# Performance work log

Hardware: AMD Instinct MI355X
Metric: run time of the kernel (lower is better)

The kernel has to match this reference:

```python
import jax, jax.numpy as jnp
import numpy as np

N = 50000      # nodes
E = 800000     # edges (before self-loops)
IN = 256
HID = 256
OUT = 128
D = 4
K = 4
K1 = 8
NUM_KS = K1 * ((1 << K) - 1)   # 120 centroids
S = HID // D                   # sub-dim per quantization slice
TAU = 1.0


def setup_inputs() -> dict:
    key = jax.random.key(0)
    ks = jax.random.split(key, 9)
    x = jax.random.normal(ks[0], (N, IN), jnp.float32)
    edge_index = jax.random.randint(ks[1], (2, E), 0, N, dtype=jnp.int64)
    def lin(k, fan_in, fan_out):
        return jax.random.normal(k, (fan_in, fan_out), jnp.float32) / np.float32(np.sqrt(fan_in))
    W0 = lin(ks[2], IN, HID); b0 = jnp.zeros((HID,), jnp.float32)
    W1 = lin(ks[3], HID, HID); b1 = jnp.zeros((HID,), jnp.float32)
    W2 = lin(ks[4], HID, OUT); b2 = jnp.zeros((OUT,), jnp.float32)
    # kaiming_normal on (NUM_KS, HID): std = sqrt(2 / fan_in), fan_in = HID
    centroids = jax.random.normal(ks[5], (NUM_KS, HID), jnp.float32) * np.float32(np.sqrt(2.0 / HID))
    return dict(x=x, edge_index=edge_index, W0=W0, b0=b0, W1=W1, b1=b1, W2=W2, b2=b2,
                centroids=centroids)


def gcn_conv(x, W, b, src, dst):
    # PyG GCNConv: add self-loops, symmetric normalization, aggregate at target
    n = x.shape[0]
    loops = jnp.arange(n, dtype=src.dtype)
    s2 = jnp.concatenate([src, loops])
    d2 = jnp.concatenate([dst, loops])
    deg = jax.ops.segment_sum(jnp.ones_like(d2, x.dtype), d2, num_segments=n)
    dinv = jnp.where(deg > 0, jax.lax.rsqrt(deg), 0.0)
    norm = dinv[s2] * dinv[d2]                      # [E+n]
    xw = x @ W                                      # [n, out]
    out = jax.ops.segment_sum(xw[s2] * norm[:, None], d2, num_segments=n)
    return out + b


def quantize(H, C):
    # H: [n, HID], C: [NUM_KS, HID]
    n = H.shape[0]
    Hr = H.reshape(n, D, S)
    Cr = C.reshape(NUM_KS, D, S)
    # products[n,k,d] = sum_s H[n,d,s] * C[k,d,s]
    prods = jnp.einsum('nds,kds->nkd', Hr, Cr) / TAU   # [n, NUM_KS, D]
    soft_l, hard_l, prob_l = [], [], []
    off = 0
    d_idx = jnp.arange(D)[None, :]
    for j in range(K):                 # K fixed small groups of sizes k_1<<j
        m = K1 << j
        sl = prods[:, off:off + m, :]                  # [n, m, D]
        p = jax.nn.softmax(sl, axis=1)                 # scatter_softmax within group
        Cg = Cr[off:off + m]                           # [m, D, S]
        soft_l.append(jnp.einsum('nmd,mds->nds', p, Cg))
        idx = jnp.argmax(sl, axis=1)                   # [n, D] scatter_max within group
        hard_l.append(Cg[idx, d_idx, :])               # [n, D, S]
        prob_l.append(p)
        off += m
    soft = jnp.stack(soft_l, 1).reshape(n, K, HID)
    hard = jnp.stack(hard_l, 1).reshape(n, K, HID)
    q = jax.lax.stop_gradient(hard - soft) + soft      # straight-through
    balance = jnp.concatenate(prob_l, 1).sum(0) / n    # [NUM_KS, D]
    k_blns = jnp.concatenate([jnp.full((K1 << j,), 1.0 / (K1 << j), jnp.float32) for j in range(K)])
    target = jnp.broadcast_to(k_blns[:, None], (NUM_KS, D))
    reg = jnp.linalg.norm(balance - target)
    pred = jnp.max(q, axis=1)                          # [n, HID]
    return pred, reg


def reference(x, edge_index, W0, b0, W1, b1, W2, b2, centroids):
    src, dst = edge_index[0], edge_index[1]
    h = jax.nn.leaky_relu(gcn_conv(x, W0, b0, src, dst), negative_slope=0.5)
    h = jax.nn.leaky_relu(gcn_conv(h, W1, b1, src, dst), negative_slope=0.5)
    pred, reg = quantize(h, centroids)
    h = h + pred
    out = gcn_conv(h, W2, b2, src, dst)
    return out, reg
```

## Files before the change

### kernel.cpp

```cpp
#include <hip/hip_runtime.h>
#include <math.h>



__global__ void k_init(int* cnt, int* cursor, int* counter, float* balance, int n) {
    int i = blockIdx.x * blockDim.x + threadIdx.x;
    if (i < n) { cnt[i] = 0; cursor[i] = 0; }
    if (i < 480) balance[i] = 0.f;
    if (i == 0) *counter = 0;
}

__global__ void k_count(const int* __restrict__ dst, int* __restrict__ cnt, int e) {
    int i = blockIdx.x * blockDim.x + threadIdx.x;
    if (i < e) atomicAdd(&cnt[dst[i]], 1);
}

__global__ void k_dinv(const int* __restrict__ cnt, float* __restrict__ dinv, int n) {
    int i = blockIdx.x * blockDim.x + threadIdx.x;
    if (i < n) dinv[i] = rsqrtf((float)cnt[i] + 1.0f);
}

__global__ void k_alloc(const int* __restrict__ cnt, int* __restrict__ row_start,
                        int* __restrict__ counter, int n) {
    int i = blockIdx.x * blockDim.x + threadIdx.x;
    if (i < n) row_start[i] = atomicAdd(counter, cnt[i]);
}

__global__ void k_fill(const int* __restrict__ src, const int* __restrict__ dst,
                       const float* __restrict__ dinv, const int* __restrict__ row_start,
                       int* __restrict__ cursor, int* __restrict__ csr_src,
                       float* __restrict__ csr_norm, int e) {
    int i = blockIdx.x * blockDim.x + threadIdx.x;
    if (i >= e) return;
    int s = src[i], d = dst[i];
    int slot = atomicAdd(&cursor[d], 1);
    int idx = row_start[d] + slot;
    csr_src[idx] = s;
    csr_norm[idx] = dinv[s] * dinv[d];
}


typedef short bf16x8 __attribute__((ext_vector_type(8)));
typedef float f32x4 __attribute__((ext_vector_type(4)));

__device__ __forceinline__ unsigned short bf16_rne(float a) {
    unsigned u = __builtin_bit_cast(unsigned, a);
    return (unsigned short)((u + 0x7FFFu + ((u >> 16) & 1u)) >> 16);
}
__device__ __forceinline__ float bf16_to_f(unsigned short h) {
    return __builtin_bit_cast(float, (unsigned)h << 16);
}

__global__ __launch_bounds__(256, 3) void k_gemm_mfma(const float* __restrict__ A,
                                                      const float* __restrict__ B,
                                                      float* __restrict__ C,
                                                      int M, int N) {
    constexpr int K = 256;
    __shared__ unsigned short Ash[128 * 40];
    __shared__ unsigned short Asl[128 * 40];
    __shared__ unsigned short Bsh[128 * 40];
    __shared__ unsigned short Bsl[128 * 40];
    const int tid = threadIdx.x;
    const int bm = blockIdx.x * 128;
    const int bn = blockIdx.y * 128;
    const int wave = tid >> 6, lane = tid & 63;
    const int wr = wave >> 1, wc = wave & 1;
    const int lr = lane & 15, lk = lane >> 4;

    f32x4 acc[4][4] = {};

    for (int k0 = 0; k0 < K; k0 += 32) {
#pragma unroll
        for (int it = 0; it < 4; ++it) {
            int q = it * 256 + tid;
            int row = q >> 3, kq = q & 7;
            float4 v = make_float4(0.f, 0.f, 0.f, 0.f);
            if (bm + row < M) v = *(const float4*)(A + (size_t)(bm + row) * K + k0 + kq * 4);
            float e[4] = {v.x, v.y, v.z, v.w};
            unsigned hh[4], ll[4];
#pragma unroll
            for (int t = 0; t < 4; ++t) {
                unsigned short h = bf16_rne(e[t]);
                unsigned short l = bf16_rne(e[t] - bf16_to_f(h));
                hh[t] = h; ll[t] = l;
            }
            unsigned off = row * 40 + kq * 4;
            *(uint2*)&Ash[off] = make_uint2(hh[0] | (hh[1] << 16), hh[2] | (hh[3] << 16));
            *(uint2*)&Asl[off] = make_uint2(ll[0] | (ll[1] << 16), ll[2] | (ll[3] << 16));
        }
#pragma unroll
        for (int it = 0; it < 4; ++it) {
            int q = it * 256 + tid;
            int k = q >> 5, nq = q & 31;
            float4 v = *(const float4*)(B + (size_t)(k0 + k) * N + bn + nq * 4);
            float e[4] = {v.x, v.y, v.z, v.w};
#pragma unroll
            for (int t = 0; t < 4; ++t) {
                unsigned short h = bf16_rne(e[t]);
                unsigned short l = bf16_rne(e[t] - bf16_to_f(h));
                Bsh[(nq * 4 + t) * 40 + k] = h;
                Bsl[(nq * 4 + t) * 40 + k] = l;
            }
        }
        __syncthreads();

        bf16x8 ah[4], al[4], bh[4], bl[4];
#pragma unroll
        for (int i = 0; i < 4; ++i) {
            unsigned off = (wr * 64 + i * 16 + lr) * 40 + lk * 8;
            ah[i] = *(bf16x8*)&Ash[off];
            al[i] = *(bf16x8*)&Asl[off];
        }
#pragma unroll
        for (int j = 0; j < 4; ++j) {
            unsigned off = (wc * 64 + j * 16 + lr) * 40 + lk * 8;
            bh[j] = *(bf16x8*)&Bsh[off];
            bl[j] = *(bf16x8*)&Bsl[off];
        }
#pragma unroll
        for (int i = 0; i < 4; ++i)
#pragma unroll
            for (int j = 0; j < 4; ++j) {
                acc[i][j] = __builtin_amdgcn_mfma_f32_16x16x32_bf16(al[i], bh[j], acc[i][j], 0, 0, 0);
                acc[i][j] = __builtin_amdgcn_mfma_f32_16x16x32_bf16(ah[i], bl[j], acc[i][j], 0, 0, 0);
                acc[i][j] = __builtin_amdgcn_mfma_f32_16x16x32_bf16(ah[i], bh[j], acc[i][j], 0, 0, 0);
            }
        __syncthreads();
    }

#pragma unroll
    for (int i = 0; i < 4; ++i) {
        int rbase = bm + wr * 64 + i * 16 + lk * 4;
#pragma unroll
        for (int r = 0; r < 4; ++r) {
            int row = rbase + r;
            if (row < M) {
#pragma unroll
                for (int j = 0; j < 4; ++j)
                    C[(size_t)row * N + bn + wc * 64 + j * 16 + lr] = acc[i][j][r];
            }
        }
    }
}


template <bool RELU>
__global__ __launch_bounds__(256, 4) void k_agg4(const float* __restrict__ xw,
                                                 const float* __restrict__ dinv,
                                                 const int* __restrict__ csr_src,
                                                 const float* __restrict__ csr_norm,
                                                 const int* __restrict__ row_start,
                                                 const int* __restrict__ cnt,
                                                 const float* __restrict__ bias,
                                                 float* __restrict__ out, int n) {
    int node = blockIdx.x * 4 + (threadIdx.x >> 6);
    if (node >= n) return;
    int lane = threadIdx.x & 63;
    int c = lane * 4;
    float di = dinv[node];
    float4 self = *(const float4*)(xw + (size_t)node * 256 + c);
    float4 bv = *(const float4*)(bias + c);
    float sw = di * di;
    float ax = self.x * sw + bv.x;
    float ay = self.y * sw + bv.y;
    float az = self.z * sw + bv.z;
    float aw = self.w * sw + bv.w;
    int st = row_start[node];
    int m = cnt[node];
    for (int t0 = 0; t0 < m; t0 += 64) {
        int rem = m - t0;
        int cnt_i = rem < 64 ? rem : 64;
        int idx_l = 0;
        float nrm_l = 0.f;
        if (lane < cnt_i) {
            idx_l = csr_src[st + t0 + lane];
            nrm_l = csr_norm[st + t0 + lane];
        }
        int t = 0;
        for (; t + 8 <= cnt_i; t += 8) {
            const float* p0 = xw + (size_t)__shfl(idx_l, t + 0, 64) * 256 + c;
            const float* p1 = xw + (size_t)__shfl(idx_l, t + 1, 64) * 256 + c;
            const float* p2 = xw + (size_t)__shfl(idx_l, t + 2, 64) * 256 + c;
            const float* p3 = xw + (size_t)__shfl(idx_l, t + 3, 64) * 256 + c;
            const float* p4 = xw + (size_t)__shfl(idx_l, t + 4, 64) * 256 + c;
            const float* p5 = xw + (size_t)__shfl(idx_l, t + 5, 64) * 256 + c;
            const float* p6 = xw + (size_t)__shfl(idx_l, t + 6, 64) * 256 + c;
            const float* p7 = xw + (size_t)__shfl(idx_l, t + 7, 64) * 256 + c;
            float4 v0 = *(const float4*)p0;
            float4 v1 = *(const float4*)p1;
            float4 v2 = *(const float4*)p2;
            float4 v3 = *(const float4*)p3;
            float4 v4 = *(const float4*)p4;
            float4 v5 = *(const float4*)p5;
            float4 v6 = *(const float4*)p6;
            float4 v7 = *(const float4*)p7;
            float w0 = __shfl(nrm_l, t + 0, 64);
            float w1 = __shfl(nrm_l, t + 1, 64);
            float w2 = __shfl(nrm_l, t + 2, 64);
            float w3 = __shfl(nrm_l, t + 3, 64);
            float w4 = __shfl(nrm_l, t + 4, 64);
            float w5 = __shfl(nrm_l, t + 5, 64);
            float w6 = __shfl(nrm_l, t + 6, 64);
            float w7 = __shfl(nrm_l, t + 7, 64);
            ax += v0.x * w0; ay += v0.y * w0; az += v0.z * w0; aw += v0.w * w0;
            ax += v1.x * w1; ay += v1.y * w1; az += v1.z * w1; aw += v1.w * w1;
            ax += v2.x * w2; ay += v2.y * w2; az += v2.z * w2; aw += v2.w * w2;
            ax += v3.x * w3; ay += v3.y * w3; az += v3.z * w3; aw += v3.w * w3;
            ax += v4.x * w4; ay += v4.y * w4; az += v4.z * w4; aw += v4.w * w4;
            ax += v5.x * w5; ay += v5.y * w5; az += v5.z * w5; aw += v5.w * w5;
            ax += v6.x * w6; ay += v6.y * w6; az += v6.z * w6; aw += v6.w * w6;
            ax += v7.x * w7; ay += v7.y * w7; az += v7.z * w7; aw += v7.w * w7;
        }
        for (; t < cnt_i; ++t) {
            int s = __shfl(idx_l, t, 64);
            float w = __shfl(nrm_l, t, 64);
            float4 v = *(const float4*)(xw + (size_t)s * 256 + c);
            ax += v.x * w; ay += v.y * w; az += v.z * w; aw += v.w * w;
        }
    }
    if (RELU) {
        ax = ax > 0.f ? ax : 0.5f * ax;
        ay = ay > 0.f ? ay : 0.5f * ay;
        az = az > 0.f ? az : 0.5f * az;
        aw = aw > 0.f ? aw : 0.5f * aw;
    }
    *(float4*)(out + (size_t)node * 256 + c) = make_float4(ax, ay, az, aw);
}

__global__ __launch_bounds__(256, 4) void k_agg2(const float* __restrict__ xw,
                                                 const float* __restrict__ dinv,
                                                 const int* __restrict__ csr_src,
                                                 const float* __restrict__ csr_norm,
                                                 const int* __restrict__ row_start,
                                                 const int* __restrict__ cnt,
                                                 const float* __restrict__ bias,
                                                 float* __restrict__ out, int n) {
    int node = blockIdx.x * 4 + (threadIdx.x >> 6);
    if (node >= n) return;
    int lane = threadIdx.x & 63;
    int c = lane * 2;
    float di = dinv[node];
    float2 self = *(const float2*)(xw + (size_t)node * 128 + c);
    float2 bv = *(const float2*)(bias + c);
    float sw = di * di;
    float ax = self.x * sw + bv.x;
    float ay = self.y * sw + bv.y;
    int st = row_start[node];
    int m = cnt[node];
    for (int t0 = 0; t0 < m; t0 += 64) {
        int rem = m - t0;
        int cnt_i = rem < 64 ? rem : 64;
        int idx_l = 0;
        float nrm_l = 0.f;
        if (lane < cnt_i) {
            idx_l = csr_src[st + t0 + lane];
            nrm_l = csr_norm[st + t0 + lane];
        }
        int t = 0;
        for (; t + 8 <= cnt_i; t += 8) {
            const float* p0 = xw + (size_t)__shfl(idx_l, t + 0, 64) * 128 + c;
            const float* p1 = xw + (size_t)__shfl(idx_l, t + 1, 64) * 128 + c;
            const float* p2 = xw + (size_t)__shfl(idx_l, t + 2, 64) * 128 + c;
            const float* p3 = xw + (size_t)__shfl(idx_l, t + 3, 64) * 128 + c;
            const float* p4 = xw + (size_t)__shfl(idx_l, t + 4, 64) * 128 + c;
            const float* p5 = xw + (size_t)__shfl(idx_l, t + 5, 64) * 128 + c;
            const float* p6 = xw + (size_t)__shfl(idx_l, t + 6, 64) * 128 + c;
            const float* p7 = xw + (size_t)__shfl(idx_l, t + 7, 64) * 128 + c;
            float2 v0 = *(const float2*)p0;
            float2 v1 = *(const float2*)p1;
            float2 v2 = *(const float2*)p2;
            float2 v3 = *(const float2*)p3;
            float2 v4 = *(const float2*)p4;
            float2 v5 = *(const float2*)p5;
            float2 v6 = *(const float2*)p6;
            float2 v7 = *(const float2*)p7;
            float w0 = __shfl(nrm_l, t + 0, 64);
            float w1 = __shfl(nrm_l, t + 1, 64);
            float w2 = __shfl(nrm_l, t + 2, 64);
            float w3 = __shfl(nrm_l, t + 3, 64);
            float w4 = __shfl(nrm_l, t + 4, 64);
            float w5 = __shfl(nrm_l, t + 5, 64);
            float w6 = __shfl(nrm_l, t + 6, 64);
            float w7 = __shfl(nrm_l, t + 7, 64);
            ax += v0.x * w0; ay += v0.y * w0;
            ax += v1.x * w1; ay += v1.y * w1;
            ax += v2.x * w2; ay += v2.y * w2;
            ax += v3.x * w3; ay += v3.y * w3;
            ax += v4.x * w4; ay += v4.y * w4;
            ax += v5.x * w5; ay += v5.y * w5;
            ax += v6.x * w6; ay += v6.y * w6;
            ax += v7.x * w7; ay += v7.y * w7;
        }
        for (; t < cnt_i; ++t) {
            int s = __shfl(idx_l, t, 64);
            float w = __shfl(nrm_l, t, 64);
            float2 v = *(const float2*)(xw + (size_t)s * 128 + c);
            ax += v.x * w; ay += v.y * w;
        }
    }
    *(float2*)(out + (size_t)node * 128 + c) = make_float2(ax, ay);
}


__global__ __launch_bounds__(256, 4) void k_quant4(const float* __restrict__ h2,
                                                   const float* __restrict__ cent,
                                                   float* __restrict__ h3,
                                                   float* __restrict__ balance_g, int n) {
    __shared__ float As[32 * 132];
    __shared__ float Bs[32 * 132];
    __shared__ float bal4[4 * 128];
    __shared__ int km_ls[128 * 4];
    const int tid = threadIdx.x;
    const int n0 = blockIdx.x * 128;
    const int d = blockIdx.y;
    const int ty = tid >> 4, tx = tid & 15;
    const int wave = tid >> 6, lane = tid & 63;

    int gid, base, sz;
    if (tx == 0)       { gid = 0; base = 0;  sz = 1; }
    else if (tx <= 2)  { gid = 1; base = 1;  sz = 2; }
    else if (tx <= 6)  { gid = 2; base = 3;  sz = 4; }
    else if (tx <= 14) { gid = 3; base = 7;  sz = 8; }
    else               { gid = 0; base = 15; sz = 0; }
    const int l = tx - base;
    const int segbase = lane & 48;

    {
        int k = tid >> 3, r = tid & 7;
        int col = (r < 4) ? (60 + r) : (120 + r);
        Bs[k * 132 + col] = 0.f;
    }

    float acc[8][8] = {};
    for (int c0 = 0; c0 < 64; c0 += 32) {
#pragma unroll
        for (int it = 0; it < 4; ++it) {
            int q = it * 256 + tid;
            int row = q >> 3, k4 = q & 7;
            float4 v = make_float4(0.f, 0.f, 0.f, 0.f);
            if (n0 + row < n)
                v = *(const float4*)(h2 + (size_t)(n0 + row) * 256 + d * 64 + c0 + k4 * 4);
            As[(k4 * 4 + 0) * 132 + row] = v.x;
            As[(k4 * 4 + 1) * 132 + row] = v.y;
            As[(k4 * 4 + 2) * 132 + row] = v.z;
            As[(k4 * 4 + 3) * 132 + row] = v.w;
        }
#pragma unroll
        for (int it = 0; it < 4; ++it) {
            int q = it * 256 + tid;
            if (q < 960) {
                int c = q >> 3, k4 = q & 7;
                float4 v = *(const float4*)(cent + (size_t)c * 256 + d * 64 + c0 + k4 * 4);
                int col = ((c >> 3) << 2) + (((c >> 2) & 1) << 6) + (c & 3);
                Bs[(k4 * 4 + 0) * 132 + col] = v.x;
                Bs[(k4 * 4 + 1) * 132 + col] = v.y;
                Bs[(k4 * 4 + 2) * 132 + col] = v.z;
                Bs[(k4 * 4 + 3) * 132 + col] = v.w;
            }
        }
        __syncthreads();
#pragma unroll 4
        for (int k = 0; k < 32; ++k) {
            float4 a0 = *(const float4*)&As[k * 132 + ty * 8];
            float4 a1 = *(const float4*)&As[k * 132 + ty * 8 + 4];
            float4 b0 = *(const float4*)&Bs[k * 132 + tx * 4];
            float4 b1 = *(const float4*)&Bs[k * 132 + 64 + tx * 4];
            float av[8] = {a0.x, a0.y, a0.z, a0.w, a1.x, a1.y, a1.z, a1.w};
            float bv[8] = {b0.x, b0.y, b0.z, b0.w, b1.x, b1.y, b1.z, b1.w};
#pragma unroll
            for (int i = 0; i < 8; ++i)
#pragma unroll
                for (int j = 0; j < 8; ++j)
                    acc[i][j] += av[i] * bv[j];
        }
        __syncthreads();
    }

    float balp[8] = {};
#pragma unroll
    for (int i = 0; i < 8; ++i) {
        const int node = ty * 8 + i;
        const bool act = (n0 + node) < n;
        float m = acc[i][0];
        int am = tx * 8;
#pragma unroll
        for (int j = 1; j < 8; ++j)
            if (acc[i][j] > m) { m = acc[i][j]; am = tx * 8 + j; }
#pragma unroll
        for (int s = 1; s <= 4; s <<= 1) {
            int pl = l ^ s;
            int srcl = segbase + base + pl;
            float mo = __shfl(m, srcl, 64);
            int amo = __shfl(am, srcl, 64);
            if (pl < sz && (mo > m || (mo == m && amo < am))) { m = mo; am = amo; }
        }
        float Z = 0.f;
#pragma unroll
        for (int j = 0; j < 8; ++j) {
            float e2 = expf(acc[i][j] - m);
            acc[i][j] = e2;
            Z += e2;
        }
#pragma unroll
        for (int s = 1; s <= 4; s <<= 1) {
            int pl = l ^ s;
            int srcl = segbase + base + pl;
            float Zo = __shfl(Z, srcl, 64);
            if (pl < sz) Z += Zo;
        }
        float invZ = (act && sz > 0) ? (1.0f / Z) : 0.f;
#pragma unroll
        for (int j = 0; j < 8; ++j) balp[j] += acc[i][j] * invZ;
        if (l == 0 && sz > 0) km_ls[node * 4 + gid] = am;
    }

#pragma unroll
    for (int j = 0; j < 8; ++j) {
        float v = balp[j];
        v += __shfl_xor(v, 16, 64);
        v += __shfl_xor(v, 32, 64);
        balp[j] = v;
    }
    if (lane < 16) {
#pragma unroll
        for (int j = 0; j < 8; ++j)
            bal4[wave * 128 + tx * 8 + j] = balp[j];
    }
    __syncthreads();
    if (tid < 120) {
        float s = bal4[tid] + bal4[128 + tid] + bal4[256 + tid] + bal4[384 + tid];
        atomicAdd(&balance_g[tid * 4 + d], s);
    }

    {
        const int node = tid >> 1;
        const int half = tid & 1;
        if (n0 + node < n) {
            int k0 = km_ls[node * 4 + 0], k1 = km_ls[node * 4 + 1];
            int k2 = km_ls[node * 4 + 2], k3 = km_ls[node * 4 + 3];
            const float* hp = h2 + (size_t)(n0 + node) * 256 + d * 64 + half * 32;
            const float* c0 = cent + (size_t)k0 * 256 + d * 64 + half * 32;
            const float* c1 = cent + (size_t)k1 * 256 + d * 64 + half * 32;
            const float* c2 = cent + (size_t)k2 * 256 + d * 64 + half * 32;
            const float* c3 = cent + (size_t)k3 * 256 + d * 64 + half * 32;
            float* op = h3 + (size_t)(n0 + node) * 256 + d * 64 + half * 32;
#pragma unroll
            for (int q = 0; q < 8; ++q) {
                int g = q * 4;
                float4 hv = *(const float4*)(hp + g);
                float4 v0 = *(const float4*)(c0 + g);
                float4 v1 = *(const float4*)(c1 + g);
                float4 v2 = *(const float4*)(c2 + g);
                float4 v3 = *(const float4*)(c3 + g);
                float4 r;
                r.x = hv.x + fmaxf(fmaxf(v0.x, v1.x), fmaxf(v2.x, v3.x));
                r.y = hv.y + fmaxf(fmaxf(v0.y, v1.y), fmaxf(v2.y, v3.y));
                r.z = hv.z + fmaxf(fmaxf(v0.z, v1.z), fmaxf(v2.z, v3.z));
                r.w = hv.w + fmaxf(fmaxf(v0.w, v1.w), fmaxf(v2.w, v3.w));
                *(float4*)(op + g) = r;
            }
        }
    }
}

__global__ void k_reg(const float* __restrict__ balance_g, float* __restrict__ out_reg,
                      float inv_n) {
    __shared__ float red[512];
    int tid = threadIdx.x;
    float v = 0.f;
    if (tid < 480) {
        int k = tid >> 2;
        float target = (k < 8) ? 0.125f : (k < 24) ? 0.0625f : (k < 56) ? 0.03125f : 0.015625f;
        float b = balance_g[tid] * inv_n;
        float df = b - target;
        v = df * df;
    }
    red[tid] = v;
    __syncthreads();
    for (int s = 256; s > 0; s >>= 1) {
        if (tid < s) red[tid] += red[tid + s];
        __syncthreads();
    }
    if (tid == 0) *out_reg = sqrtf(red[0]);
}


extern "C" void kernel_launch(void* const* d_in, const int* in_sizes, int n_in,
                              void* d_out, int out_size, void* d_ws, size_t ws_size,
                              hipStream_t stream) {
    const float* x    = (const float*)d_in[0];
    const int*   ei   = (const int*)d_in[1];
    const float* W0   = (const float*)d_in[2];
    const float* b0   = (const float*)d_in[3];
    const float* W1   = (const float*)d_in[4];
    const float* b1   = (const float*)d_in[5];
    const float* W2   = (const float*)d_in[6];
    const float* b2   = (const float*)d_in[7];
    const float* cent = (const float*)d_in[8];
    const int n = in_sizes[0] / 256;
    const int e = in_sizes[1] / 2;
    const int* src = ei;
    const int* dst = ei + e;
    float* out = (float*)d_out;

    char* w = (char*)d_ws;
    float* bufA = (float*)w;      w += (size_t)n * 256 * 4;
    float* bufB = (float*)w;      w += (size_t)n * 256 * 4;
    float* dinv = (float*)w;      w += (size_t)n * 4;
    int* cnt = (int*)w;           w += (size_t)n * 4;
    int* row_start = (int*)w;     w += (size_t)n * 4;
    int* cursor = (int*)w;        w += (size_t)n * 4;
    int* csr_src = (int*)w;       w += (size_t)e * 4;
    float* csr_norm = (float*)w;  w += (size_t)e * 4;
    int* counter = (int*)w;       w += 256;
    float* balance = (float*)w;   w += 480 * 4;

    const int tb = 256;
    k_init<<<(n + tb - 1) / tb, tb, 0, stream>>>(cnt, cursor, counter, balance, n);
    k_count<<<(e + tb - 1) / tb, tb, 0, stream>>>(dst, cnt, e);
    k_dinv<<<(n + tb - 1) / tb, tb, 0, stream>>>(cnt, dinv, n);
    k_alloc<<<(n + tb - 1) / tb, tb, 0, stream>>>(cnt, row_start, counter, n);
    k_fill<<<(e + tb - 1) / tb, tb, 0, stream>>>(src, dst, dinv, row_start, cursor,
                                                 csr_src, csr_norm, e);

    dim3 g1((n + 127) / 128, 2);
    k_gemm_mfma<<<g1, 256, 0, stream>>>(x, W0, bufA, n, 256);
    k_agg4<true><<<(n + 3) / 4, 256, 0, stream>>>(bufA, dinv, csr_src, csr_norm,
                                                  row_start, cnt, b0, bufB, n);
    k_gemm_mfma<<<g1, 256, 0, stream>>>(bufB, W1, bufA, n, 256);
    k_agg4<true><<<(n + 3) / 4, 256, 0, stream>>>(bufA, dinv, csr_src, csr_norm,
                                                  row_start, cnt, b1, bufB, n);

    dim3 gq((n + 127) / 128, 4);
    k_quant4<<<gq, 256, 0, stream>>>(bufB, cent, bufA, balance, n);

    dim3 g3((n + 127) / 128, 1);
    k_gemm_mfma<<<g3, 256, 0, stream>>>(bufA, W2, bufB, n, 128);
    k_agg2<<<(n + 3) / 4, 256, 0, stream>>>(bufB, dinv, csr_src, csr_norm,
                                            row_start, cnt, b2, out, n);
    k_reg<<<1, 512, 0, stream>>>(balance, out + (size_t)n * 128, 1.0f / (float)n);
}
```

Measured before the change: 723.7 us.

## Pre-split GEMM operands into bf16 hi/lo arrays in producer kernels

Moves the fp32-to-bf16 hi/lo splitting out of the GEMM inner loop. Weights are pre-transposed and split once, x is split by a separate kernel, and the aggregation and quantize kernels write hi/lo bf16 outputs directly for the next GEMM. The GEMM now loads bf16x8 vectors straight into padded shared memory, with no per-tile conversion and no strided transpose stores for B. In exchange it adds extra kernel launches and an extra pass over x. The A-operand traffic stays roughly the same, since hi and lo together take as many bytes as fp32.

```diff
diff --git a/kernel.cpp b/kernel.cpp
--- a/kernel.cpp
+++ b/kernel.cpp
@@ -1,6 +1,24 @@
 #include <hip/hip_runtime.h>
 #include <math.h>
 
+
+typedef short bf16x8 __attribute__((ext_vector_type(8)));
+typedef float f32x4 __attribute__((ext_vector_type(4)));
+
+__device__ __forceinline__ unsigned short bf16_rne(float a) {
+    unsigned u = __builtin_bit_cast(unsigned, a);
+    return (unsigned short)((u + 0x7FFFu + ((u >> 16) & 1u)) >> 16);
+}
+__device__ __forceinline__ float bf16_to_f(unsigned short h) {
+    return __builtin_bit_cast(float, (unsigned)h << 16);
+}
+__device__ __forceinline__ void split4(const float* e, unsigned short* h, unsigned short* l) {
+#pragma unroll
+    for (int t = 0; t < 4; ++t) {
+        h[t] = bf16_rne(e[t]);
+        l[t] = bf16_rne(e[t] - bf16_to_f(h[t]));
+    }
+}
 
 
 __global__ void k_init(int* cnt, int* cursor, int* counter, float* balance, int n) {
@@ -40,26 +58,42 @@
 }
 
 
-typedef short bf16x8 __attribute__((ext_vector_type(8)));
-typedef float f32x4 __attribute__((ext_vector_type(4)));
-
-__device__ __forceinline__ unsigned short bf16_rne(float a) {
-    unsigned u = __builtin_bit_cast(unsigned, a);
-    return (unsigned short)((u + 0x7FFFu + ((u >> 16) & 1u)) >> 16);
-}
-__device__ __forceinline__ float bf16_to_f(unsigned short h) {
-    return __builtin_bit_cast(float, (unsigned)h << 16);
-}
-
-__global__ __launch_bounds__(256, 3) void k_gemm_mfma(const float* __restrict__ A,
-                                                      const float* __restrict__ B,
-                                                      float* __restrict__ C,
-                                                      int M, int N) {
-    constexpr int K = 256;
-    __shared__ unsigned short Ash[128 * 40];
-    __shared__ unsigned short Asl[128 * 40];
-    __shared__ unsigned short Bsh[128 * 40];
-    __shared__ unsigned short Bsl[128 * 40];
+__global__ void k_splitW(const float* __restrict__ W, short* __restrict__ Th,
+                         short* __restrict__ Tl, int N) {
+    int i = blockIdx.x * blockDim.x + threadIdx.x;
+    if (i >= N * 256) return;
+    int nn = i >> 8, kk = i & 255;
+    float v = W[kk * N + nn];
+    unsigned short h = bf16_rne(v);
+    unsigned short l = bf16_rne(v - bf16_to_f(h));
+    Th[i] = (short)h;
+    Tl[i] = (short)l;
+}
+
+__global__ void k_splitA(const float* __restrict__ X, short* __restrict__ Hi,
+                         short* __restrict__ Lo, int total8) {
+    int i = blockIdx.x * blockDim.x + threadIdx.x;
+    if (i >= total8) return;
+    float4 a = *(const float4*)(X + (size_t)i * 8);
+    float4 b = *(const float4*)(X + (size_t)i * 8 + 4);
+    float e0[4] = {a.x, a.y, a.z, a.w}, e1[4] = {b.x, b.y, b.z, b.w};
+    unsigned short h0[4], l0[4], h1[4], l1[4];
+    split4(e0, h0, l0);
+    split4(e1, h1, l1);
+    *(uint4*)(Hi + (size_t)i * 8) = make_uint4(h0[0] | (h0[1] << 16), h0[2] | (h0[3] << 16),
+                                              h1[0] | (h1[1] << 16), h1[2] | (h1[3] << 16));
+    *(uint4*)(Lo + (size_t)i * 8) = make_uint4(l0[0] | (l0[1] << 16), l0[2] | (l0[3] << 16),
+                                              l1[0] | (l1[1] << 16), l1[2] | (l1[3] << 16));
+}
+
+
+__global__ __launch_bounds__(256, 2) void k_gemm_bf16s(const short* __restrict__ Ah,
+                                                       const short* __restrict__ Al,
+                                                       const short* __restrict__ Bh,
+                                                       const short* __restrict__ Bl,
+                                                       float* __restrict__ C,
+                                                       int M, int N) {
+    __shared__ short Ash[128 * 56], Asl[128 * 56], Bsh[128 * 56], Bsl[128 * 56];
     const int tid = threadIdx.x;
     const int bm = blockIdx.x * 128;
     const int bn = blockIdx.y * 128;
@@ -69,51 +103,37 @@
 
     f32x4 acc[4][4] = {};
 
-    for (int k0 = 0; k0 < K; k0 += 32) {
-#pragma unroll
-        for (int it = 0; it < 4; ++it) {
-            int q = it * 256 + tid;
-            int row = q >> 3, kq = q & 7;
-            float4 v = make_float4(0.f, 0.f, 0.f, 0.f);
-            if (bm + row < M) v = *(const float4*)(A + (size_t)(bm + row) * K + k0 + kq * 4);
-            float e[4] = {v.x, v.y, v.z, v.w};
-            unsigned hh[4], ll[4];
-#pragma unroll
-            for (int t = 0; t < 4; ++t) {
-                unsigned short h = bf16_rne(e[t]);
-                unsigned short l = bf16_rne(e[t] - bf16_to_f(h));
-                hh[t] = h; ll[t] = l;
+    for (int k0 = 0; k0 < 256; k0 += 32) {
+#pragma unroll
+        for (int it = 0; it < 2; ++it) {
+            int u = it * 256 + tid;
+            int row = u >> 2, sg = (u & 3) << 3;
+            int lo_off = row * 56 + sg;
+            size_t arow = (size_t)(bm + row) * 256 + k0 + sg;
+            bf16x8 va = {0, 0, 0, 0, 0, 0, 0, 0};
+            bf16x8 vl = {0, 0, 0, 0, 0, 0, 0, 0};
+            if (bm + row < M) {
+                va = *(const bf16x8*)(Ah + arow);
+                vl = *(const bf16x8*)(Al + arow);
             }
-            unsigned off = row * 40 + kq * 4;
-            *(uint2*)&Ash[off] = make_uint2(hh[0] | (hh[1] << 16), hh[2] | (hh[3] << 16));
-            *(uint2*)&Asl[off] = make_uint2(ll[0] | (ll[1] << 16), ll[2] | (ll[3] << 16));
-        }
-#pragma unroll
-        for (int it = 0; it < 4; ++it) {
-            int q = it * 256 + tid;
-            int k = q >> 5, nq = q & 31;
-            float4 v = *(const float4*)(B + (size_t)(k0 + k) * N + bn + nq * 4);
-            float e[4] = {v.x, v.y, v.z, v.w};
-#pragma unroll
-            for (int t = 0; t < 4; ++t) {
-                unsigned short h = bf16_rne(e[t]);
-                unsigned short l = bf16_rne(e[t] - bf16_to_f(h));
-                Bsh[(nq * 4 + t) * 40 + k] = h;
-                Bsl[(nq * 4 + t) * 40 + k] = l;
-            }
+            *(bf16x8*)&Ash[lo_off] = va;
+            *(bf16x8*)&Asl[lo_off] = vl;
+            size_t brow = (size_t)(bn + row) * 256 + k0 + sg;
+            *(bf16x8*)&Bsh[lo_off] = *(const bf16x8*)(Bh + brow);
+            *(bf16x8*)&Bsl[lo_off] = *(const bf16x8*)(Bl + brow);
         }
         __syncthreads();
 
         bf16x8 ah[4], al[4], bh[4], bl[4];
 #pragma unroll
         for (int i = 0; i < 4; ++i) {
-            unsigned off = (wr * 64 + i * 16 + lr) * 40 + lk * 8;
+            int off = (wr * 64 + i * 16 + lr) * 56 + lk * 8;
             ah[i] = *(bf16x8*)&Ash[off];
             al[i] = *(bf16x8*)&Asl[off];
         }
 #pragma unroll
         for (int j = 0; j < 4; ++j) {
-            unsigned off = (wc * 64 + j * 16 + lr) * 40 + lk * 8;
+            int off = (wc * 64 + j * 16 + lr) * 56 + lk * 8;
             bh[j] = *(bf16x8*)&Bsh[off];
             bl[j] = *(bf16x8*)&Bsl[off];
         }
@@ -144,7 +164,7 @@
 }
 
 
-template <bool RELU>
+template <bool RELU, int MODE>
 __global__ __launch_bounds__(256, 4) void k_agg4(const float* __restrict__ xw,
                                                  const float* __restrict__ dinv,
                                                  const int* __restrict__ csr_src,
@@ -152,7 +172,9 @@
                                                  const int* __restrict__ row_start,
                                                  const int* __restrict__ cnt,
                                                  const float* __restrict__ bias,
-                                                 float* __restrict__ out, int n) {
+                                                 float* __restrict__ out,
+                                                 short* __restrict__ outH,
+                                                 short* __restrict__ outL, int n) {
     int node = blockIdx.x * 4 + (threadIdx.x >> 6);
     if (node >= n) return;
     int lane = threadIdx.x & 63;
@@ -224,7 +246,16 @@
         az = az > 0.f ? az : 0.5f * az;
         aw = aw > 0.f ? aw : 0.5f * aw;
     }
-    *(float4*)(out + (size_t)node * 256 + c) = make_float4(ax, ay, az, aw);
+    if (MODE == 0) {
+        *(float4*)(out + (size_t)node * 256 + c) = make_float4(ax, ay, az, aw);
+    } else {
+        float e[4] = {ax, ay, az, aw};
+        unsigned short h[4], l[4];
+        split4(e, h, l);
+        size_t o = (size_t)node * 256 + c;
+        *(uint2*)(outH + o) = make_uint2(h[0] | (h[1] << 16), h[2] | (h[3] << 16));
+        *(uint2*)(outL + o) = make_uint2(l[0] | (l[1] << 16), l[2] | (l[3] << 16));
+    }
 }
 
 __global__ __launch_bounds__(256, 4) void k_agg2(const float* __restrict__ xw,
@@ -304,7 +335,8 @@
 
 __global__ __launch_bounds__(256, 4) void k_quant4(const float* __restrict__ h2,
                                                    const float* __restrict__ cent,
-                                                   float* __restrict__ h3,
+                                                   short* __restrict__ h3h,
+                                                   short* __restrict__ h3l,
                                                    float* __restrict__ balance_g, int n) {
     __shared__ float As[32 * 132];
     __shared__ float Bs[32 * 132];
@@ -443,7 +475,7 @@
             const float* c1 = cent + (size_t)k1 * 256 + d * 64 + half * 32;
             const float* c2 = cent + (size_t)k2 * 256 + d * 64 + half * 32;
             const float* c3 = cent + (size_t)k3 * 256 + d * 64 + half * 32;
-            float* op = h3 + (size_t)(n0 + node) * 256 + d * 64 + half * 32;
+            size_t obase = (size_t)(n0 + node) * 256 + d * 64 + half * 32;
 #pragma unroll
             for (int q = 0; q < 8; ++q) {
                 int g = q * 4;
@@ -452,12 +484,15 @@
                 float4 v1 = *(const float4*)(c1 + g);
                 float4 v2 = *(const float4*)(c2 + g);
                 float4 v3 = *(const float4*)(c3 + g);
-                float4 r;
-                r.x = hv.x + fmaxf(fmaxf(v0.x, v1.x), fmaxf(v2.x, v3.x));
-                r.y = hv.y + fmaxf(fmaxf(v0.y, v1.y), fmaxf(v2.y, v3.y));
-                r.z = hv.z + fmaxf(fmaxf(v0.z, v1.z), fmaxf(v2.z, v3.z));
-                r.w = hv.w + fmaxf(fmaxf(v0.w, v1.w), fmaxf(v2.w, v3.w));
-                *(float4*)(op + g) = r;
+                float e[4];
+                e[0] = hv.x + fmaxf(fmaxf(v0.x, v1.x), fmaxf(v2.x, v3.x));
+                e[1] = hv.y + fmaxf(fmaxf(v0.y, v1.y), fmaxf(v2.y, v3.y));
+                e[2] = hv.z + fmaxf(fmaxf(v0.z, v1.z), fmaxf(v2.z, v3.z));
+                e[3] = hv.w + fmaxf(fmaxf(v0.w, v1.w), fmaxf(v2.w, v3.w));
+                unsigned short h[4], l[4];
+                split4(e, h, l);
+                *(uint2*)(h3h + obase + g) = make_uint2(h[0] | (h[1] << 16), h[2] | (h[3] << 16));
+                *(uint2*)(h3l + obase + g) = make_uint2(l[0] | (l[1] << 16), l[2] | (l[3] << 16));
             }
         }
     }
@@ -514,6 +549,19 @@
     float* csr_norm = (float*)w;  w += (size_t)e * 4;
     int* counter = (int*)w;       w += 256;
     float* balance = (float*)w;   w += 480 * 4;
+    short* w0h = (short*)w;       w += 256 * 256 * 2;
+    short* w0l = (short*)w;       w += 256 * 256 * 2;
+    short* w1h = (short*)w;       w += 256 * 256 * 2;
+    short* w1l = (short*)w;       w += 256 * 256 * 2;
+    short* w2h = (short*)w;       w += 128 * 256 * 2;
+    short* w2l = (short*)w;       w += 128 * 256 * 2;
+
+    short* xh = (short*)bufA;
+    short* xl = xh + (size_t)n * 256;
+    short* h1h = (short*)bufA;
+    short* h1l = h1h + (size_t)n * 256;
+    short* h3h = (short*)bufB;
+    short* h3l = h3h + (size_t)n * 256;
 
     const int tb = 256;
     k_init<<<(n + tb - 1) / tb, tb, 0, stream>>>(cnt, cursor, counter, balance, n);
@@ -523,20 +571,27 @@
     k_fill<<<(e + tb - 1) / tb, tb, 0, stream>>>(src, dst, dinv, row_start, cursor,
                                                  csr_src, csr_norm, e);
 
+    k_splitW<<<(256 * 256 + tb - 1) / tb, tb, 0, stream>>>(W0, w0h, w0l, 256);
+    k_splitW<<<(256 * 256 + tb - 1) / tb, tb, 0, stream>>>(W1, w1h, w1l, 256);
+    k_splitW<<<(128 * 256 + tb - 1) / tb, tb, 0, stream>>>(W2, w2h, w2l, 128);
+    k_splitA<<<(n * 32 + tb - 1) / tb, tb, 0, stream>>>(x, xh, xl, n * 32);
+
     dim3 g1((n + 127) / 128, 2);
-    k_gemm_mfma<<<g1, 256, 0, stream>>>(x, W0, bufA, n, 256);
-    k_agg4<true><<<(n + 3) / 4, 256, 0, stream>>>(bufA, dinv, csr_src, csr_norm,
-                                                  row_start, cnt, b0, bufB, n);
-    k_gemm_mfma<<<g1, 256, 0, stream>>>(bufB, W1, bufA, n, 256);
-    k_agg4<true><<<(n + 3) / 4, 256, 0, stream>>>(bufA, dinv, csr_src, csr_norm,
-                                                  row_start, cnt, b1, bufB, n);
+    k_gemm_bf16s<<<g1, 256, 0, stream>>>(xh, xl, w0h, w0l, bufB, n, 256);
+    k_agg4<true, 1><<<(n + 3) / 4, 256, 0, stream>>>(bufB, dinv, csr_src, csr_norm,
+                                                     row_start, cnt, b0, nullptr,
+                                                     h1h, h1l, n);
+    k_gemm_bf16s<<<g1, 256, 0, stream>>>(h1h, h1l, w1h, w1l, bufB, n, 256);
+    k_agg4<true, 0><<<(n + 3) / 4, 256, 0, stream>>>(bufB, dinv, csr_src, csr_norm,
+                                                     row_start, cnt, b1, bufA,
+                                                     nullptr, nullptr, n);
 
     dim3 gq((n + 127) / 128, 4);
-    k_quant4<<<gq, 256, 0, stream>>>(bufB, cent, bufA, balance, n);
+    k_quant4<<<gq, 256, 0, stream>>>(bufA, cent, h3h, h3l, balance, n);
 
     dim3 g3((n + 127) / 128, 1);
-    k_gemm_mfma<<<g3, 256, 0, stream>>>(bufA, W2, bufB, n, 128);
-    k_agg2<<<(n + 3) / 4, 256, 0, stream>>>(bufB, dinv, csr_src, csr_norm,
+    k_gemm_bf16s<<<g3, 256, 0, stream>>>(h3h, h3l, w2h, w2l, bufA, n, 128);
+    k_agg2<<<(n + 3) / 4, 256, 0, stream>>>(bufA, dinv, csr_src, csr_norm,
                                             row_start, cnt, b2, out, n);
     k_reg<<<1, 512, 0, stream>>>(balance, out + (size_t)n * 128, 1.0f / (float)n);
 }
```

After: 619.6 us. 1.17x faster.
